# Kernel optimization log

Measured on AMD Instinct MI355X. Metric: run time of the kernel, lower is better.

The kernel has to match this reference:

```python
import jax, jax.numpy as jnp
import numpy as np

H = W = 32
K = 3


def _im2col(a):
    # a: [B, C, H, W] -> patches [B, H*W, C*K*K], channel-major (c, kh, kw)
    # matching torch.nn.Unfold ordering.
    a_pad = jnp.pad(a, ((0, 0), (0, 0), (1, 1), (1, 1)), mode='reflect')  # [B,C,H+2,W+2]
    cols = jnp.stack(
        [a_pad[:, :, kh:kh + H, kw:kw + W] for kh in range(K) for kw in range(K)],
        axis=2,
    )  # [B, C, 9, H, W]
    B, C = a.shape[0], a.shape[1]
    cols = cols.reshape(B, C * K * K, H * W)  # [B, 576, 1024]
    return jnp.swapaxes(cols, 1, 2)  # [B, 1024, 576]


def setup_inputs() -> dict:
    key = jax.random.key(0)
    k1, k2 = jax.random.split(key)
    a = jax.random.normal(k1, (256, 64, 32, 32), dtype=jnp.float32)
    # kaiming_uniform fan_in = 576 -> bound = sqrt(6/576)
    bound = float(np.sqrt(6.0 / 576.0))
    conv_kernel = jax.random.uniform(k2, (576, 64), dtype=jnp.float32,
                                     minval=-bound, maxval=bound)
    return {"a": a, "conv_kernel": conv_kernel}


def reference(a, conv_kernel):
    patches = _im2col(a)  # [B, 1024, 576]
    mean = jnp.mean(patches, axis=-1, keepdims=True)
    std = jnp.std(patches, axis=-1, keepdims=True, ddof=1)  # torch unbiased std
    normed = (patches - mean) / std
    out = jnp.einsum('blp,po->blo', normed, conv_kernel)  # [B, 1024, 64]
    # Fold with 1x1 kernel == reshape back to [B, 64, 32, 32]
    out = jnp.swapaxes(out, 1, 2).reshape(a.shape[0], conv_kernel.shape[1], H, W)
    return out
```

## Files before the change

kernel.cpp:

```cpp
#include <hip/hip_runtime.h>


#define STRIDE 68
#define NPIX   544

typedef __attribute__((ext_vector_type(8))) short bf16x8;
typedef __attribute__((ext_vector_type(4))) short bf16x4;
typedef __attribute__((ext_vector_type(4))) float f32x4;

__device__ __forceinline__ unsigned short f2bf(float f) {
    union { float f; unsigned u; } v; v.f = f;
    unsigned r = v.u + 0x7FFFu + ((v.u >> 16) & 1u);
    return (unsigned short)(r >> 16);
}

__device__ __forceinline__ int reflect32(int x) {
    x = (x < 0) ? -x : x;
    return (x > 31) ? (62 - x) : x;
}

__global__ void reorder_w_kernel(const float* __restrict__ W, uint4* __restrict__ wf) {
    int idx = blockIdx.x * 256 + threadIdx.x;
    if (idx >= 4608) return;
    int lane = idx & 63;
    int ks   = (idx >> 6) % 18;
    int ntg  = idx / 1152;
    int quad = lane >> 4;
    int o    = ntg * 16 + (lane & 15);
    unsigned short v[8];
    #pragma unroll
    for (int j = 0; j < 8; ++j) {
        int kp = ks * 32 + quad * 8 + j;
        int c  = kp & 63;
        int s  = kp >> 6;
        v[j] = f2bf(W[(c * 9 + s) * 64 + o]);
    }
    uint4 r;
    r.x = (unsigned)v[0] | ((unsigned)v[1] << 16);
    r.y = (unsigned)v[2] | ((unsigned)v[3] << 16);
    r.z = (unsigned)v[4] | ((unsigned)v[5] << 16);
    r.w = (unsigned)v[6] | ((unsigned)v[7] << 16);
    wf[idx] = r;
}

__global__ __launch_bounds__(256, 2)
void norm_conv_kernel(const float* __restrict__ a,
                      const uint4* __restrict__ wf,
                      float* __restrict__ out) {
    __shared__ unsigned short img[NPIX * STRIDE];
    __shared__ float sums[1088];

    const int tid  = threadIdx.x;
    const int b    = blockIdx.x >> 1;
    const int half = blockIdx.x & 1;
    const int row_base = half * 15;
    const int lane = tid & 63;
    const int wid  = tid >> 6;
    const int ng   = wid & 1;
    const int wq   = wid >> 1;
    const int quad = lane >> 4;
    const int mlan = lane & 15;

    bf16x8 bfrag[2][18];
    #pragma unroll
    for (int nt = 0; nt < 2; ++nt) {
        #pragma unroll
        for (int ks = 0; ks < 18; ++ks) {
            union { uint4 u; bf16x8 v; } cvt;
            cvt.u = wf[((ng * 2 + nt) * 18 + ks) * 64 + lane];
            bfrag[nt][ks] = cvt.v;
        }
    }

    const float* Ab = a + (size_t)b * 65536 + row_base * 32;
    for (int p = tid; p < NPIX; p += 256) {
        float s = 0.f, q = 0.f;
        unsigned short* row = &img[p * STRIDE];
        #pragma unroll 8
        for (int c = 0; c < 64; c += 2) {
            float v0 = Ab[c * 1024 + p];
            float v1 = Ab[(c + 1) * 1024 + p];
            s += v0 + v1;
            q += v0 * v0 + v1 * v1;
            unsigned pk = (unsigned)f2bf(v0) | ((unsigned)f2bf(v1) << 16);
            *(unsigned*)&row[c] = pk;
        }
        sums[p] = s;
        sums[NPIX + p] = q;
    }
    __syncthreads();

    float mean_[2], inv_[2];
    #pragma unroll
    for (int i = 0; i < 2; ++i) {
        int lo = tid + i * 256;
        int hg = half * 16 + (lo >> 5);
        int wg = lo & 31;
        float s = 0.f, q = 0.f;
        #pragma unroll
        for (int kh = 0; kh < 3; ++kh) {
            int hr = reflect32(hg + kh - 1) - row_base;
            #pragma unroll
            for (int kw = 0; kw < 3; ++kw) {
                int p = hr * 32 + reflect32(wg + kw - 1);
                s += sums[p];
                q += sums[NPIX + p];
            }
        }
        float mean = s * (1.0f / 576.0f);
        float var  = (q - s * mean) * (1.0f / 575.0f);
        mean_[i] = mean;
        inv_[i]  = rsqrtf(var);
    }
    __syncthreads();
    #pragma unroll
    for (int i = 0; i < 2; ++i) {
        int lo = tid + i * 256;
        sums[lo * 2]     = mean_[i];
        sums[lo * 2 + 1] = inv_[i];
    }
    __syncthreads();

    float So[2];
    #pragma unroll
    for (int nt = 0; nt < 2; ++nt) {
        float s = 0.f;
        #pragma unroll
        for (int ks = 0; ks < 18; ++ks) {
            #pragma unroll
            for (int j = 0; j < 8; ++j) {
                union { unsigned u; float f; } cv;
                cv.u = ((unsigned)(unsigned short)bfrag[nt][ks][j]) << 16;
                s += cv.f;
            }
        }
        s += __shfl_xor(s, 16, 64);
        s += __shfl_xor(s, 32, 64);
        So[nt] = s;
    }

    float* outB = out + (size_t)b * 65536 + half * 512;
    const char* imgc = (const char*)img;
    for (int i = 0; i < 16; ++i) {
        int mt = wq * 16 + i;
        int hg = half * 16 + (mt >> 1);
        int wl = ((mt & 1) << 4) + mlan;
        int base9[9];
        #pragma unroll
        for (int kh = 0; kh < 3; ++kh) {
            int pr = (reflect32(hg + kh - 1) - row_base) * 32;
            #pragma unroll
            for (int kw = 0; kw < 3; ++kw) {
                base9[kh * 3 + kw] = ((pr + reflect32(wl + kw - 1)) * STRIDE + quad * 8) * 2;
            }
        }
        f32x4 acc0 = {0.f, 0.f, 0.f, 0.f};
        f32x4 acc1 = {0.f, 0.f, 0.f, 0.f};
        #pragma unroll
        for (int ks = 0; ks < 18; ++ks) {
            int off = base9[ks >> 1] + (ks & 1) * 64;
            bf16x4 flo = *(const bf16x4*)(imgc + off);
            bf16x4 fhi = *(const bf16x4*)(imgc + off + 8);
            bf16x8 af  = __builtin_shufflevector(flo, fhi, 0, 1, 2, 3, 4, 5, 6, 7);
            acc0 = __builtin_amdgcn_mfma_f32_16x16x32_bf16(af, bfrag[0][ks], acc0, 0, 0, 0);
            acc1 = __builtin_amdgcn_mfma_f32_16x16x32_bf16(af, bfrag[1][ks], acc1, 0, 0, 0);
        }
        int l0 = mt * 16 + quad * 4;
        f32x4 r0, r1;
        #pragma unroll
        for (int r = 0; r < 4; ++r) {
            float mean = sums[(l0 + r) * 2];
            float inv  = sums[(l0 + r) * 2 + 1];
            r0[r] = (acc0[r] - mean * So[0]) * inv;
            r1[r] = (acc1[r] - mean * So[1]) * inv;
        }
        int o0 = ng * 32 + mlan;
        *(f32x4*)(outB + o0 * 1024 + l0) = r0;
        *(f32x4*)(outB + (o0 + 16) * 1024 + l0) = r1;
    }
}

extern "C" void kernel_launch(void* const* d_in, const int* in_sizes, int n_in,
                              void* d_out, int out_size, void* d_ws, size_t ws_size,
                              hipStream_t stream) {
    const float* a = (const float*)d_in[0];
    const float* w = (const float*)d_in[1];
    float* out = (float*)d_out;
    uint4* wf = (uint4*)d_ws;
    reorder_w_kernel<<<dim3(18), dim3(256), 0, stream>>>(w, wf);
    norm_conv_kernel<<<dim3(512), dim3(256), 0, stream>>>(a, (const uint4*)wf, out);
}
```

Before: 127.1 us.

## Split each image into four row-quarter blocks and stream weights from global memory

The conv kernel now runs 1024 blocks of 512 threads, each covering 8 output rows with a 10-row halo, instead of 512 blocks covering 16 rows. Each wave computes one row across all 64 output channels, streaming the bf16 weight fragments from global/L2 with a one-step prefetch instead of holding them all in registers. The per-output-channel weight sums are moved into a prep block. The aim is higher occupancy and better latency hiding, at the cost of more halo rows reloaded per image and repeated weight fetches from cache.

```diff
diff --git a/kernel.cpp b/kernel.cpp
--- a/kernel.cpp
+++ b/kernel.cpp
@@ -2,7 +2,8 @@
 
 
 #define STRIDE 68
-#define NPIX   544
+#define NROW   10
+#define NPIX   320
 
 typedef __attribute__((ext_vector_type(8))) short bf16x8;
 typedef __attribute__((ext_vector_type(4))) short bf16x4;
@@ -19,9 +20,24 @@
     return (x > 31) ? (62 - x) : x;
 }
 
-__global__ void reorder_w_kernel(const float* __restrict__ W, uint4* __restrict__ wf) {
+__global__ void prep_kernel(const float* __restrict__ W, uint4* __restrict__ wf,
+                            float* __restrict__ scolg) {
+    if (blockIdx.x == 18) {
+        __shared__ float red[256];
+        int t = threadIdx.x;
+        int o = t & 63, kq = t >> 6;
+        float s = 0.f;
+        for (int k = kq * 144; k < kq * 144 + 144; ++k) {
+            union { unsigned u; float f; } cv;
+            cv.u = ((unsigned)f2bf(W[k * 64 + o])) << 16;
+            s += cv.f;
+        }
+        red[t] = s;
+        __syncthreads();
+        if (t < 64) scolg[t] = red[t] + red[t + 64] + red[t + 128] + red[t + 192];
+        return;
+    }
     int idx = blockIdx.x * 256 + threadIdx.x;
-    if (idx >= 4608) return;
     int lane = idx & 63;
     int ks   = (idx >> 6) % 18;
     int ntg  = idx / 1152;
@@ -43,140 +59,141 @@
     wf[idx] = r;
 }
 
-__global__ __launch_bounds__(256, 2)
+__global__ __launch_bounds__(512, 4)
 void norm_conv_kernel(const float* __restrict__ a,
                       const uint4* __restrict__ wf,
+                      const float* __restrict__ scolg,
                       float* __restrict__ out) {
     __shared__ unsigned short img[NPIX * STRIDE];
-    __shared__ float sums[1088];
-
-    const int tid  = threadIdx.x;
-    const int b    = blockIdx.x >> 1;
-    const int half = blockIdx.x & 1;
-    const int row_base = half * 15;
+    __shared__ float sums[2 * NPIX];
+
+    const int tid = threadIdx.x;
+    const int b   = blockIdx.x >> 2;
+    const int q   = blockIdx.x & 3;
+    const int row_base = (q == 0) ? 0 : (q == 3 ? 22 : 8 * q - 1);
     const int lane = tid & 63;
     const int wid  = tid >> 6;
-    const int ng   = wid & 1;
-    const int wq   = wid >> 1;
     const int quad = lane >> 4;
     const int mlan = lane & 15;
 
-    bf16x8 bfrag[2][18];
-    #pragma unroll
-    for (int nt = 0; nt < 2; ++nt) {
-        #pragma unroll
-        for (int ks = 0; ks < 18; ++ks) {
-            union { uint4 u; bf16x8 v; } cvt;
-            cvt.u = wf[((ng * 2 + nt) * 18 + ks) * 64 + lane];
-            bfrag[nt][ks] = cvt.v;
-        }
-    }
-
     const float* Ab = a + (size_t)b * 65536 + row_base * 32;
-    for (int p = tid; p < NPIX; p += 256) {
-        float s = 0.f, q = 0.f;
-        unsigned short* row = &img[p * STRIDE];
-        #pragma unroll 8
-        for (int c = 0; c < 64; c += 2) {
-            float v0 = Ab[c * 1024 + p];
-            float v1 = Ab[(c + 1) * 1024 + p];
-            s += v0 + v1;
-            q += v0 * v0 + v1 * v1;
-            unsigned pk = (unsigned)f2bf(v0) | ((unsigned)f2bf(v1) << 16);
-            *(unsigned*)&row[c] = pk;
-        }
-        sums[p] = s;
-        sums[NPIX + p] = q;
+    for (int u = tid; u < 640; u += 512) {
+        int p  = u >> 1;
+        int ch = (u & 1) * 32;
+        float s = 0.f, qq = 0.f;
+        unsigned short* row = &img[p * STRIDE + ch];
+        #pragma unroll
+        for (int c4 = 0; c4 < 32; c4 += 4) {
+            float v0 = Ab[(ch + c4) * 1024 + p];
+            float v1 = Ab[(ch + c4 + 1) * 1024 + p];
+            float v2 = Ab[(ch + c4 + 2) * 1024 + p];
+            float v3 = Ab[(ch + c4 + 3) * 1024 + p];
+            s  += (v0 + v1) + (v2 + v3);
+            qq += (v0 * v0 + v1 * v1) + (v2 * v2 + v3 * v3);
+            uint2 pk;
+            pk.x = (unsigned)f2bf(v0) | ((unsigned)f2bf(v1) << 16);
+            pk.y = (unsigned)f2bf(v2) | ((unsigned)f2bf(v3) << 16);
+            *(uint2*)&row[c4] = pk;
+        }
+        s  += __shfl_xor(s, 1, 64);
+        qq += __shfl_xor(qq, 1, 64);
+        if ((u & 1) == 0) { sums[p] = s; sums[NPIX + p] = qq; }
     }
     __syncthreads();
 
-    float mean_[2], inv_[2];
-    #pragma unroll
-    for (int i = 0; i < 2; ++i) {
-        int lo = tid + i * 256;
-        int hg = half * 16 + (lo >> 5);
-        int wg = lo & 31;
-        float s = 0.f, q = 0.f;
+    float mean = 0.f, inv = 0.f;
+    if (tid < 256) {
+        int hg = q * 8 + (tid >> 5);
+        int wg = tid & 31;
+        float s = 0.f, ss = 0.f;
         #pragma unroll
         for (int kh = 0; kh < 3; ++kh) {
             int hr = reflect32(hg + kh - 1) - row_base;
             #pragma unroll
             for (int kw = 0; kw < 3; ++kw) {
                 int p = hr * 32 + reflect32(wg + kw - 1);
-                s += sums[p];
-                q += sums[NPIX + p];
+                s  += sums[p];
+                ss += sums[NPIX + p];
             }
         }
-        float mean = s * (1.0f / 576.0f);
-        float var  = (q - s * mean) * (1.0f / 575.0f);
-        mean_[i] = mean;
-        inv_[i]  = rsqrtf(var);
+        mean = s * (1.0f / 576.0f);
+        inv  = rsqrtf((ss - s * mean) * (1.0f / 575.0f));
     }
     __syncthreads();
-    #pragma unroll
-    for (int i = 0; i < 2; ++i) {
-        int lo = tid + i * 256;
-        sums[lo * 2]     = mean_[i];
-        sums[lo * 2 + 1] = inv_[i];
-    }
+    if (tid < 256) { sums[tid * 2] = mean; sums[tid * 2 + 1] = inv; }
     __syncthreads();
 
-    float So[2];
-    #pragma unroll
-    for (int nt = 0; nt < 2; ++nt) {
-        float s = 0.f;
-        #pragma unroll
-        for (int ks = 0; ks < 18; ++ks) {
-            #pragma unroll
-            for (int j = 0; j < 8; ++j) {
-                union { unsigned u; float f; } cv;
-                cv.u = ((unsigned)(unsigned short)bfrag[nt][ks][j]) << 16;
-                s += cv.f;
-            }
-        }
-        s += __shfl_xor(s, 16, 64);
-        s += __shfl_xor(s, 32, 64);
-        So[nt] = s;
-    }
-
-    float* outB = out + (size_t)b * 65536 + half * 512;
+    float So[4];
+    #pragma unroll
+    for (int nt = 0; nt < 4; ++nt) So[nt] = scolg[nt * 16 + mlan];
+
+    int rowb[3], colb[2][3];
+    #pragma unroll
+    for (int kh = 0; kh < 3; ++kh)
+        rowb[kh] = (reflect32(q * 8 + wid + kh - 1) - row_base) * (32 * STRIDE * 2) + quad * 16;
+    #pragma unroll
+    for (int j = 0; j < 2; ++j)
+        #pragma unroll
+        for (int kw = 0; kw < 3; ++kw)
+            colb[j][kw] = reflect32(j * 16 + mlan + kw - 1) * (STRIDE * 2);
+
+    f32x4 acc[2][4];
+    #pragma unroll
+    for (int mt = 0; mt < 2; ++mt)
+        #pragma unroll
+        for (int nt = 0; nt < 4; ++nt)
+            acc[mt][nt] = (f32x4){0.f, 0.f, 0.f, 0.f};
+
+    const uint4* bp = wf + lane;
+    uint4 bnx[4];
+    #pragma unroll
+    for (int nt = 0; nt < 4; ++nt) bnx[nt] = bp[nt * 18 * 64];
+
     const char* imgc = (const char*)img;
-    for (int i = 0; i < 16; ++i) {
-        int mt = wq * 16 + i;
-        int hg = half * 16 + (mt >> 1);
-        int wl = ((mt & 1) << 4) + mlan;
-        int base9[9];
-        #pragma unroll
-        for (int kh = 0; kh < 3; ++kh) {
-            int pr = (reflect32(hg + kh - 1) - row_base) * 32;
-            #pragma unroll
-            for (int kw = 0; kw < 3; ++kw) {
-                base9[kh * 3 + kw] = ((pr + reflect32(wl + kw - 1)) * STRIDE + quad * 8) * 2;
-            }
-        }
-        f32x4 acc0 = {0.f, 0.f, 0.f, 0.f};
-        f32x4 acc1 = {0.f, 0.f, 0.f, 0.f};
-        #pragma unroll
-        for (int ks = 0; ks < 18; ++ks) {
-            int off = base9[ks >> 1] + (ks & 1) * 64;
+    #pragma unroll
+    for (int ks = 0; ks < 18; ++ks) {
+        uint4 bc[4];
+        #pragma unroll
+        for (int nt = 0; nt < 4; ++nt) bc[nt] = bnx[nt];
+        if (ks < 17) {
+            #pragma unroll
+            for (int nt = 0; nt < 4; ++nt) bnx[nt] = bp[(nt * 18 + ks + 1) * 64];
+        }
+        const int khi = (ks >> 1) / 3;
+        const int kwi = (ks >> 1) % 3;
+        const int coff = (ks & 1) * 64;
+        #pragma unroll
+        for (int mt = 0; mt < 2; ++mt) {
+            int off = rowb[khi] + colb[mt][kwi] + coff;
             bf16x4 flo = *(const bf16x4*)(imgc + off);
             bf16x4 fhi = *(const bf16x4*)(imgc + off + 8);
             bf16x8 af  = __builtin_shufflevector(flo, fhi, 0, 1, 2, 3, 4, 5, 6, 7);
-            acc0 = __builtin_amdgcn_mfma_f32_16x16x32_bf16(af, bfrag[0][ks], acc0, 0, 0, 0);
-            acc1 = __builtin_amdgcn_mfma_f32_16x16x32_bf16(af, bfrag[1][ks], acc1, 0, 0, 0);
-        }
-        int l0 = mt * 16 + quad * 4;
-        f32x4 r0, r1;
+            #pragma unroll
+            for (int nt = 0; nt < 4; ++nt) {
+                union { uint4 u; bf16x8 v; } cb; cb.u = bc[nt];
+                acc[mt][nt] = __builtin_amdgcn_mfma_f32_16x16x32_bf16(af, cb.v, acc[mt][nt], 0, 0, 0);
+            }
+        }
+    }
+
+    float* outB = out + (size_t)b * 65536 + q * 256;
+    #pragma unroll
+    for (int mt = 0; mt < 2; ++mt) {
+        int l0 = (wid * 2 + mt) * 16 + quad * 4;
+        float mn[4], iv[4];
         #pragma unroll
         for (int r = 0; r < 4; ++r) {
-            float mean = sums[(l0 + r) * 2];
-            float inv  = sums[(l0 + r) * 2 + 1];
-            r0[r] = (acc0[r] - mean * So[0]) * inv;
-            r1[r] = (acc1[r] - mean * So[1]) * inv;
-        }
-        int o0 = ng * 32 + mlan;
-        *(f32x4*)(outB + o0 * 1024 + l0) = r0;
-        *(f32x4*)(outB + (o0 + 16) * 1024 + l0) = r1;
+            mn[r] = sums[(l0 + r) * 2];
+            iv[r] = sums[(l0 + r) * 2 + 1];
+        }
+        #pragma unroll
+        for (int nt = 0; nt < 4; ++nt) {
+            f32x4 rr;
+            #pragma unroll
+            for (int r = 0; r < 4; ++r)
+                rr[r] = (acc[mt][nt][r] - mn[r] * So[nt]) * iv[r];
+            *(f32x4*)(outB + (nt * 16 + mlan) * 1024 + l0) = rr;
+        }
     }
 }
 
@@ -187,6 +204,7 @@
     const float* w = (const float*)d_in[1];
     float* out = (float*)d_out;
     uint4* wf = (uint4*)d_ws;
-    reorder_w_kernel<<<dim3(18), dim3(256), 0, stream>>>(w, wf);
-    norm_conv_kernel<<<dim3(512), dim3(256), 0, stream>>>(a, (const uint4*)wf, out);
-}
+    float* scolg = (float*)((char*)d_ws + 73728);
+    prep_kernel<<<dim3(19), dim3(256), 0, stream>>>(w, wf, scolg);
+    norm_conv_kernel<<<dim3(1024), dim3(512), 0, stream>>>(a, wf, scolg, out);
+}
```

Result: slower. 153.0 us (+20.3%).

## Process whole image per block with double-buffered row-strip staging

Applied to the files above, without the earlier changes.

Each block of 512 threads now handles one full image in four 8-row strips (10 rows staged with halo), instead of two blocks each staging a 17-row half. Global loads for the next strip are issued into registers before the MFMA loop on the current strip, then committed to a second LDS buffer, so load latency overlaps compute. The column sums of the bf16 weights move into the prep kernel, and per-pixel stats are now computed from the bf16-rounded LDS values. The trade-off is fewer blocks (256), more barriers, a 40-float register staging buffer that raises register pressure, and a small change in numerics.

```diff
diff --git a/kernel.cpp b/kernel.cpp
--- a/kernel.cpp
+++ b/kernel.cpp
@@ -2,7 +2,7 @@
 
 
 #define STRIDE 68
-#define NPIX   544
+#define NPIX   320
 
 typedef __attribute__((ext_vector_type(8))) short bf16x8;
 typedef __attribute__((ext_vector_type(4))) short bf16x4;
@@ -14,14 +14,31 @@
     return (unsigned short)(r >> 16);
 }
 
+__device__ __forceinline__ float bf2f(unsigned short h) {
+    union { unsigned u; float f; } v; v.u = ((unsigned)h) << 16;
+    return v.f;
+}
+
 __device__ __forceinline__ int reflect32(int x) {
     x = (x < 0) ? -x : x;
     return (x > 31) ? (62 - x) : x;
 }
 
-__global__ void reorder_w_kernel(const float* __restrict__ W, uint4* __restrict__ wf) {
+__global__ void prep_kernel(const float* __restrict__ W, uint4* __restrict__ wf,
+                            float* __restrict__ scolg) {
+    if (blockIdx.x == 18) {
+        __shared__ float red[256];
+        int t = threadIdx.x;
+        int o = t & 63, kq = t >> 6;
+        float s = 0.f;
+        for (int k = kq * 144; k < kq * 144 + 144; ++k)
+            s += bf2f(f2bf(W[k * 64 + o]));
+        red[t] = s;
+        __syncthreads();
+        if (t < 64) scolg[t] = red[t] + red[t + 64] + red[t + 128] + red[t + 192];
+        return;
+    }
     int idx = blockIdx.x * 256 + threadIdx.x;
-    if (idx >= 4608) return;
     int lane = idx & 63;
     int ks   = (idx >> 6) % 18;
     int ntg  = idx / 1152;
@@ -43,17 +60,46 @@
     wf[idx] = r;
 }
 
-__global__ __launch_bounds__(256, 2)
+__device__ __constant__ int c_rb[4] = {0, 7, 15, 22};
+
+__device__ __forceinline__ void stage_issue(const float* __restrict__ Ab,
+                                            int tid, float* vals) {
+    #pragma unroll
+    for (int k = 0; k < 10; ++k) {
+        int u  = tid + 512 * k;
+        int c4 = u / 320;
+        int p  = u - c4 * 320;
+        #pragma unroll
+        for (int j = 0; j < 4; ++j)
+            vals[k * 4 + j] = Ab[(c4 * 4 + j) * 1024 + p];
+    }
+}
+
+__device__ __forceinline__ void stage_commit(unsigned short* __restrict__ imgb,
+                                             int tid, const float* vals) {
+    #pragma unroll
+    for (int k = 0; k < 10; ++k) {
+        int u  = tid + 512 * k;
+        int c4 = u / 320;
+        int p  = u - c4 * 320;
+        uint2 pk;
+        pk.x = (unsigned)f2bf(vals[k * 4 + 0]) | ((unsigned)f2bf(vals[k * 4 + 1]) << 16);
+        pk.y = (unsigned)f2bf(vals[k * 4 + 2]) | ((unsigned)f2bf(vals[k * 4 + 3]) << 16);
+        *(uint2*)&imgb[p * STRIDE + c4 * 4] = pk;
+    }
+}
+
+__global__ __launch_bounds__(512, 2)
 void norm_conv_kernel(const float* __restrict__ a,
                       const uint4* __restrict__ wf,
+                      const float* __restrict__ scolg,
                       float* __restrict__ out) {
-    __shared__ unsigned short img[NPIX * STRIDE];
-    __shared__ float sums[1088];
+    __shared__ unsigned short img[2][NPIX * STRIDE];
+    __shared__ float sums[2 * NPIX];
+    __shared__ float stats[2][512];
 
     const int tid  = threadIdx.x;
-    const int b    = blockIdx.x >> 1;
-    const int half = blockIdx.x & 1;
-    const int row_base = half * 15;
+    const int b    = blockIdx.x;
     const int lane = tid & 63;
     const int wid  = tid >> 6;
     const int ng   = wid & 1;
@@ -63,120 +109,148 @@
 
     bf16x8 bfrag[2][18];
     #pragma unroll
-    for (int nt = 0; nt < 2; ++nt) {
+    for (int nt = 0; nt < 2; ++nt)
         #pragma unroll
         for (int ks = 0; ks < 18; ++ks) {
             union { uint4 u; bf16x8 v; } cvt;
             cvt.u = wf[((ng * 2 + nt) * 18 + ks) * 64 + lane];
             bfrag[nt][ks] = cvt.v;
         }
-    }
-
-    const float* Ab = a + (size_t)b * 65536 + row_base * 32;
-    for (int p = tid; p < NPIX; p += 256) {
-        float s = 0.f, q = 0.f;
-        unsigned short* row = &img[p * STRIDE];
-        #pragma unroll 8
-        for (int c = 0; c < 64; c += 2) {
-            float v0 = Ab[c * 1024 + p];
-            float v1 = Ab[(c + 1) * 1024 + p];
-            s += v0 + v1;
-            q += v0 * v0 + v1 * v1;
-            unsigned pk = (unsigned)f2bf(v0) | ((unsigned)f2bf(v1) << 16);
-            *(unsigned*)&row[c] = pk;
-        }
-        sums[p] = s;
-        sums[NPIX + p] = q;
-    }
-    __syncthreads();
-
-    float mean_[2], inv_[2];
-    #pragma unroll
-    for (int i = 0; i < 2; ++i) {
-        int lo = tid + i * 256;
-        int hg = half * 16 + (lo >> 5);
-        int wg = lo & 31;
-        float s = 0.f, q = 0.f;
-        #pragma unroll
-        for (int kh = 0; kh < 3; ++kh) {
-            int hr = reflect32(hg + kh - 1) - row_base;
-            #pragma unroll
-            for (int kw = 0; kw < 3; ++kw) {
-                int p = hr * 32 + reflect32(wg + kw - 1);
-                s += sums[p];
-                q += sums[NPIX + p];
-            }
-        }
-        float mean = s * (1.0f / 576.0f);
-        float var  = (q - s * mean) * (1.0f / 575.0f);
-        mean_[i] = mean;
-        inv_[i]  = rsqrtf(var);
-    }
-    __syncthreads();
-    #pragma unroll
-    for (int i = 0; i < 2; ++i) {
-        int lo = tid + i * 256;
-        sums[lo * 2]     = mean_[i];
-        sums[lo * 2 + 1] = inv_[i];
-    }
-    __syncthreads();
-
     float So[2];
-    #pragma unroll
-    for (int nt = 0; nt < 2; ++nt) {
-        float s = 0.f;
-        #pragma unroll
-        for (int ks = 0; ks < 18; ++ks) {
-            #pragma unroll
-            for (int j = 0; j < 8; ++j) {
-                union { unsigned u; float f; } cv;
-                cv.u = ((unsigned)(unsigned short)bfrag[nt][ks][j]) << 16;
-                s += cv.f;
-            }
-        }
-        s += __shfl_xor(s, 16, 64);
-        s += __shfl_xor(s, 32, 64);
-        So[nt] = s;
-    }
-
-    float* outB = out + (size_t)b * 65536 + half * 512;
-    const char* imgc = (const char*)img;
-    for (int i = 0; i < 16; ++i) {
-        int mt = wq * 16 + i;
-        int hg = half * 16 + (mt >> 1);
-        int wl = ((mt & 1) << 4) + mlan;
-        int base9[9];
-        #pragma unroll
-        for (int kh = 0; kh < 3; ++kh) {
-            int pr = (reflect32(hg + kh - 1) - row_base) * 32;
-            #pragma unroll
-            for (int kw = 0; kw < 3; ++kw) {
-                base9[kh * 3 + kw] = ((pr + reflect32(wl + kw - 1)) * STRIDE + quad * 8) * 2;
-            }
-        }
-        f32x4 acc0 = {0.f, 0.f, 0.f, 0.f};
-        f32x4 acc1 = {0.f, 0.f, 0.f, 0.f};
-        #pragma unroll
-        for (int ks = 0; ks < 18; ++ks) {
-            int off = base9[ks >> 1] + (ks & 1) * 64;
-            bf16x4 flo = *(const bf16x4*)(imgc + off);
-            bf16x4 fhi = *(const bf16x4*)(imgc + off + 8);
-            bf16x8 af  = __builtin_shufflevector(flo, fhi, 0, 1, 2, 3, 4, 5, 6, 7);
-            acc0 = __builtin_amdgcn_mfma_f32_16x16x32_bf16(af, bfrag[0][ks], acc0, 0, 0, 0);
-            acc1 = __builtin_amdgcn_mfma_f32_16x16x32_bf16(af, bfrag[1][ks], acc1, 0, 0, 0);
-        }
-        int l0 = mt * 16 + quad * 4;
-        f32x4 r0, r1;
-        #pragma unroll
-        for (int r = 0; r < 4; ++r) {
-            float mean = sums[(l0 + r) * 2];
-            float inv  = sums[(l0 + r) * 2 + 1];
-            r0[r] = (acc0[r] - mean * So[0]) * inv;
-            r1[r] = (acc1[r] - mean * So[1]) * inv;
-        }
-        int o0 = ng * 32 + mlan;
-        *(f32x4*)(outB + o0 * 1024 + l0) = r0;
-        *(f32x4*)(outB + (o0 + 16) * 1024 + l0) = r1;
+    So[0] = scolg[(ng * 2 + 0) * 16 + mlan];
+    So[1] = scolg[(ng * 2 + 1) * 16 + mlan];
+
+    const float* Aimg = a + (size_t)b * 65536;
+    float* outB = out + (size_t)b * 65536;
+
+    {
+        float vals[40];
+        stage_issue(Aimg + c_rb[0] * 32, tid, vals);
+        stage_commit(img[0], tid, vals);
+        __syncthreads();
+        if (tid < NPIX) {
+            float s = 0.f, ss = 0.f;
+            const unsigned short* row = &img[0][tid * STRIDE];
+            #pragma unroll
+            for (int g = 0; g < 16; ++g) {
+                uint2 w4 = *(const uint2*)&row[g * 4];
+                float f0 = bf2f((unsigned short)(w4.x & 0xFFFF));
+                float f1 = bf2f((unsigned short)(w4.x >> 16));
+                float f2 = bf2f((unsigned short)(w4.y & 0xFFFF));
+                float f3 = bf2f((unsigned short)(w4.y >> 16));
+                s  += (f0 + f1) + (f2 + f3);
+                ss += (f0 * f0 + f1 * f1) + (f2 * f2 + f3 * f3);
+            }
+            sums[tid] = s; sums[NPIX + tid] = ss;
+        }
+        __syncthreads();
+        if (tid < 256) {
+            int hg = (tid >> 5);
+            int wg = tid & 31;
+            float s = 0.f, ss = 0.f;
+            #pragma unroll
+            for (int kh = 0; kh < 3; ++kh) {
+                int hr = reflect32(hg + kh - 1) - c_rb[0];
+                #pragma unroll
+                for (int kw = 0; kw < 3; ++kw) {
+                    int p = hr * 32 + reflect32(wg + kw - 1);
+                    s  += sums[p];
+                    ss += sums[NPIX + p];
+                }
+            }
+            float mean = s * (1.0f / 576.0f);
+            stats[0][tid * 2]     = mean;
+            stats[0][tid * 2 + 1] = rsqrtf((ss - s * mean) * (1.0f / 575.0f));
+        }
+        __syncthreads();
+    }
+
+    for (int q = 0; q < 4; ++q) {
+        const int cur = q & 1, nxt = cur ^ 1;
+        float vals[40];
+        if (q < 3)
+            stage_issue(Aimg + c_rb[q + 1] * 32, tid, vals);
+
+        const unsigned short* imgb = img[cur];
+        const char* imgc = (const char*)imgb;
+        const float* st  = stats[cur];
+        const int rb = c_rb[q];
+        for (int i = 0; i < 4; ++i) {
+            int mt = wq * 4 + i;
+            int hg = q * 8 + (mt >> 1);
+            int wl = ((mt & 1) << 4) + mlan;
+            int base9[9];
+            #pragma unroll
+            for (int kh = 0; kh < 3; ++kh) {
+                int pr = (reflect32(hg + kh - 1) - rb) * 32;
+                #pragma unroll
+                for (int kw = 0; kw < 3; ++kw)
+                    base9[kh * 3 + kw] = ((pr + reflect32(wl + kw - 1)) * STRIDE + quad * 8) * 2;
+            }
+            f32x4 acc0 = {0.f, 0.f, 0.f, 0.f};
+            f32x4 acc1 = {0.f, 0.f, 0.f, 0.f};
+            #pragma unroll
+            for (int ks = 0; ks < 18; ++ks) {
+                int off = base9[ks >> 1] + (ks & 1) * 64;
+                bf16x4 flo = *(const bf16x4*)(imgc + off);
+                bf16x4 fhi = *(const bf16x4*)(imgc + off + 8);
+                bf16x8 af  = __builtin_shufflevector(flo, fhi, 0, 1, 2, 3, 4, 5, 6, 7);
+                acc0 = __builtin_amdgcn_mfma_f32_16x16x32_bf16(af, bfrag[0][ks], acc0, 0, 0, 0);
+                acc1 = __builtin_amdgcn_mfma_f32_16x16x32_bf16(af, bfrag[1][ks], acc1, 0, 0, 0);
+            }
+            int l0 = mt * 16 + quad * 4;
+            f32x4 r0, r1;
+            #pragma unroll
+            for (int r = 0; r < 4; ++r) {
+                float mean = st[(l0 + r) * 2];
+                float inv  = st[(l0 + r) * 2 + 1];
+                r0[r] = (acc0[r] - mean * So[0]) * inv;
+                r1[r] = (acc1[r] - mean * So[1]) * inv;
+            }
+            int o0 = (ng * 2) * 16 + mlan;
+            *(f32x4*)(outB + o0 * 1024 + q * 256 + l0) = r0;
+            *(f32x4*)(outB + (o0 + 16) * 1024 + q * 256 + l0) = r1;
+        }
+
+        if (q < 3) {
+            stage_commit(img[nxt], tid, vals);
+            __syncthreads();
+            if (tid < NPIX) {
+                float s = 0.f, ss = 0.f;
+                const unsigned short* row = &img[nxt][tid * STRIDE];
+                #pragma unroll
+                for (int g = 0; g < 16; ++g) {
+                    uint2 w4 = *(const uint2*)&row[g * 4];
+                    float f0 = bf2f((unsigned short)(w4.x & 0xFFFF));
+                    float f1 = bf2f((unsigned short)(w4.x >> 16));
+                    float f2 = bf2f((unsigned short)(w4.y & 0xFFFF));
+                    float f3 = bf2f((unsigned short)(w4.y >> 16));
+                    s  += (f0 + f1) + (f2 + f3);
+                    ss += (f0 * f0 + f1 * f1) + (f2 * f2 + f3 * f3);
+                }
+                sums[tid] = s; sums[NPIX + tid] = ss;
+            }
+            __syncthreads();
+            if (tid < 256) {
+                int hg = (q + 1) * 8 + (tid >> 5);
+                int wg = tid & 31;
+                float s = 0.f, ss = 0.f;
+                #pragma unroll
+                for (int kh = 0; kh < 3; ++kh) {
+                    int hr = reflect32(hg + kh - 1) - c_rb[q + 1];
+                    #pragma unroll
+                    for (int kw = 0; kw < 3; ++kw) {
+                        int p = hr * 32 + reflect32(wg + kw - 1);
+                        s  += sums[p];
+                        ss += sums[NPIX + p];
+                    }
+                }
+                float mean = s * (1.0f / 576.0f);
+                stats[nxt][tid * 2]     = mean;
+                stats[nxt][tid * 2 + 1] = rsqrtf((ss - s * mean) * (1.0f / 575.0f));
+            }
+            __syncthreads();
+        }
     }
 }
 
@@ -187,6 +261,7 @@
     const float* w = (const float*)d_in[1];
     float* out = (float*)d_out;
     uint4* wf = (uint4*)d_ws;
-    reorder_w_kernel<<<dim3(18), dim3(256), 0, stream>>>(w, wf);
-    norm_conv_kernel<<<dim3(512), dim3(256), 0, stream>>>(a, (const uint4*)wf, out);
-}
+    float* scolg = (float*)((char*)d_ws + 73728);
+    prep_kernel<<<dim3(19), dim3(256), 0, stream>>>(w, wf, scolg);
+    norm_conv_kernel<<<dim3(256), dim3(512), 0, stream>>>(a, wf, scolg, out);
+}
```

New measurement: 330.8 us. 2.6x slower.
